# Kernel optimization log

Measured on AMD Instinct MI355X. Metric: run time of the kernel, lower is better.

Reference implementation:

```python
import jax, jax.numpy as jnp
import numpy as np

PIXEL_W = 1.0
EPS = 1e-8
BIG = 1e10


def extract_zero_crossings(s):
    """Vectorized marching-squares-style zero-crossing extraction.
    s: (H, W) SDF. Returns padded points (N, 2) float and validity mask (N,) bool,
    N = (H-1)*W + H*(W-1), in the same (vertical pairs first, then horizontal)
    order as the original python loops."""
    H, W = s.shape
    dt = s.dtype
    # vertical neighbor pairs (i, j) vs (i+1, j)
    v1, v2 = s[:-1, :], s[1:, :]
    ii = jnp.broadcast_to(jnp.arange(H - 1, dtype=dt)[:, None], (H - 1, W))
    jj = jnp.broadcast_to(jnp.arange(W, dtype=dt)[None, :], (H - 1, W))
    c1 = v1 == 0
    c2 = (~c1) & (v2 == 0)
    cx = (~c1) & (~c2) & (v1 * v2 < 0)
    alpha = jnp.abs(v1) / (jnp.abs(v1) + jnp.abs(v2) + EPS)
    row = jnp.where(c1, ii, jnp.where(c2, ii + 1.0, ii + alpha))
    pts_v = jnp.stack([row, jj], axis=-1).reshape(-1, 2)
    m_v = (c1 | c2 | cx).reshape(-1)
    # horizontal neighbor pairs (i, j) vs (i, j+1)
    h1, h2 = s[:, :-1], s[:, 1:]
    ii2 = jnp.broadcast_to(jnp.arange(H, dtype=dt)[:, None], (H, W - 1))
    jj2 = jnp.broadcast_to(jnp.arange(W - 1, dtype=dt)[None, :], (H, W - 1))
    d1 = h1 == 0
    d2 = (~d1) & (h2 == 0)
    dx = (~d1) & (~d2) & (h1 * h2 < 0)
    beta = jnp.abs(h1) / (jnp.abs(h1) + jnp.abs(h2) + EPS)
    col = jnp.where(d1, jj2, jnp.where(d2, jj2 + 1.0, jj2 + beta))
    pts_h = jnp.stack([ii2, col], axis=-1).reshape(-1, 2)
    m_h = (d1 | d2 | dx).reshape(-1)
    return jnp.concatenate([pts_v, pts_h], 0), jnp.concatenate([m_v, m_h], 0)


def pairwise_dist(p, g):
    # (Np, Ng) euclidean distances via the gram trick (avoids (Np,Ng,2) temp)
    d2 = jnp.sum(p * p, 1)[:, None] + jnp.sum(g * g, 1)[None, :] - 2.0 * (p @ g.T)
    return jnp.sqrt(jnp.maximum(d2, 0.0))


def masked_chamfer(pp, pm, gp, gm):
    # chamfer as in compute_chamfer_distance: -mean(min over gt) + mean(min over pred)
    d = pairwise_dist(pp, gp)
    d = jnp.where(pm[:, None] & gm[None, :], d, BIG)
    min_p = jnp.min(d, axis=1)
    min_g = jnp.min(d, axis=0)
    np_ = jnp.maximum(jnp.sum(pm), 1)
    ng_ = jnp.maximum(jnp.sum(gm), 1)
    return -jnp.sum(jnp.where(pm, min_p, 0.0)) / np_ + jnp.sum(jnp.where(gm, min_g, 0.0)) / ng_


def setup_inputs() -> dict:
    key = jax.random.key(0)
    k1, k2 = jax.random.split(key)
    B, H, W = 2, 80, 80
    return {
        "pred_logits": jax.random.normal(k1, (B, 1, H, W), dtype=jnp.float32),
        "gt_sdf": jax.random.normal(k2, (B, 1, H, W), dtype=jnp.float32),
    }


def reference(pred_logits, gt_sdf):
    pred = pred_logits[:, 0]  # (B, H, W)
    gt = gt_sdf[:, 0]
    pixel_loss = jnp.mean(jnp.abs(pred - gt))
    chamfers = []
    for b in range(pred.shape[0]):  # small fixed batch loop
        pp, pm = extract_zero_crossings(pred[b])
        gp, gm = extract_zero_crossings(gt[b])
        chamfers.append(masked_chamfer(pp, pm, gp, gm))
    loss = PIXEL_W * pixel_loss
    last_chamfer = jnp.mean(jnp.stack(chamfers))
    return loss, last_chamfer
```

## Files before the change

### kernel.cpp

```cpp
#include <hip/hip_runtime.h>

#define HH 80
#define WW 80
#define IMG (HH * WW)
#define NV ((HH - 1) * WW)
#define NPTS (NV + HH * (WW - 1))
#define NPIX (2 * IMG)
#define BIGF 1.0e10f
#define INVC 1.0e7f
#define EPSF 1e-8f
#define QSCALE 131072.0f

#define SETPAD 12800
#define SBLOCKS (SETPAD / 256)
#define EXBLOCKS (4 * SBLOCKS)
#define PXBLOCKS (NPIX / 256)
#define PREPB (EXBLOCKS + PXBLOCKS)

#define BLK 256
#define APT 8
#define ACHUNK (BLK * APT)
#define ABLOCKS ((NPTS + ACHUNK - 1) / ACHUNK)
#define NSLICE 32
#define MAXSLICE ((((NPTS + NSLICE - 1) / NSLICE) + 1) & ~1)

#define CNT_STRIDE 32
#define PIX_OFF 512
#define TICKET_OFF 640
#define SUM_OFF 768
#define SCALAR_BYTES 1024

__device__ __forceinline__ long long wave_reduce_ll(long long v) {
#pragma unroll
  for (int o = 32; o > 0; o >>= 1) {
    int2 p = *(int2*)&v;
    p.x = __shfl_down(p.x, o, 64);
    p.y = __shfl_down(p.y, o, 64);
    v += *(long long*)&p;
  }
  return v;
}

__global__ void k_zero(unsigned int* __restrict__ w) {
  w[threadIdx.x] = 0u;
}

__global__ void __launch_bounds__(256) k_prep(
    const float* __restrict__ pred, const float* __restrict__ gt,
    float2* __restrict__ pts, float* __restrict__ minarr,
    int* __restrict__ cnt, unsigned long long* __restrict__ pix_i) {
  __shared__ int wc[4], wo[4];
  __shared__ long long rl[4];
  int tid = threadIdx.x, lane = tid & 63, wid = tid >> 6;
  int gtid = blockIdx.x * 256 + tid;

  if (gtid < 4 * NPTS) minarr[gtid] = BIGF;

  if (blockIdx.x < EXBLOCKS) {
    int set = blockIdx.x / SBLOCKS;
    int idx = (blockIdx.x % SBLOCKS) * 256 + tid;
    const float* s = (set < 2 ? pred : gt) + (set & 1) * IMG;
    float r = 0.f, c = 0.f;
    bool valid = false;
    if (idx < NPTS) {
      if (idx < NV) {
        int i = idx / WW, j = idx - i * WW;
        float v1 = s[i * WW + j], v2 = s[(i + 1) * WW + j];
        c = (float)j;
        if (v1 == 0.f)      { r = (float)i;       valid = true; }
        else if (v2 == 0.f) { r = (float)i + 1.f; valid = true; }
        else {
          r = (float)i + fabsf(v1) / (fabsf(v1) + fabsf(v2) + EPSF);
          valid = (v1 * v2 < 0.f);
        }
      } else {
        int t = idx - NV;
        int i = t / (WW - 1), j = t - i * (WW - 1);
        float h1 = s[i * WW + j], h2 = s[i * WW + j + 1];
        r = (float)i;
        if (h1 == 0.f)      { c = (float)j;       valid = true; }
        else if (h2 == 0.f) { c = (float)j + 1.f; valid = true; }
        else {
          c = (float)j + fabsf(h1) / (fabsf(h1) + fabsf(h2) + EPSF);
          valid = (h1 * h2 < 0.f);
        }
      }
    }
    unsigned long long mask = __ballot(valid);
    int nw = __popcll(mask);
    if (lane == 0) wc[wid] = nw;
    __syncthreads();
    if (tid == 0) {
      int t0 = wc[0], t1 = wc[1], t2 = wc[2], t3 = wc[3];
      int tot = t0 + t1 + t2 + t3;
      int base = tot ? atomicAdd(&cnt[set * CNT_STRIDE], tot) : 0;
      wo[0] = base; wo[1] = base + t0; wo[2] = base + t0 + t1;
      wo[3] = base + t0 + t1 + t2;
    }
    __syncthreads();
    if (valid) {
      int lpos = __popcll(mask & ((1ull << lane) - 1ull));
      pts[set * NPTS + wo[wid] + lpos] = make_float2(r, c);
    }
  } else {
    int p = (blockIdx.x - EXBLOCKS) * 256 + tid;
    float d = fabsf(pred[p] - gt[p]);
    long long q = (long long)(d * QSCALE + 0.5f);
    q = wave_reduce_ll(q);
    if (lane == 0) rl[wid] = q;
    __syncthreads();
    if (tid == 0)
      atomicAdd(pix_i, (unsigned long long)(rl[0] + rl[1] + rl[2] + rl[3]));
  }
}

__global__ void __launch_bounds__(BLK) k_min(
    const float2* __restrict__ pts, float* __restrict__ minarr,
    const int* __restrict__ cnt) {
  int dir = blockIdx.z;
  int Aset = ((dir & 1) << 1) | (dir >> 1);
  int Bset = Aset ^ 2;
  int cntA = cnt[Aset * CNT_STRIDE], cntB = cnt[Bset * CNT_STRIDE];

  int abase0 = blockIdx.x * ACHUNK;
  if (abase0 >= cntA) return;
  int slicelen = (((cntB + NSLICE - 1) / NSLICE) + 1) & ~1;
  int b0 = blockIdx.y * slicelen;
  if (b0 >= cntB) return;
  int n = min(slicelen, cntB - b0);
  int sn = (n + 1) & ~1;

  __shared__ float4 tile[MAXSLICE];
  for (int i = threadIdx.x; i < sn; i += BLK) {
    float2 q = (i < n) ? pts[Bset * NPTS + b0 + i] : make_float2(INVC, INVC);
    tile[i] = make_float4(q.x, q.y, fmaf(q.x, q.x, q.y * q.y), 0.f);
  }
  __syncthreads();

  int abase = abase0 + threadIdx.x;
  float nx[APT], ny[APT], p2[APT], m[APT];
#pragma unroll
  for (int i = 0; i < APT; ++i) {
    int a = abase + i * BLK;
    float2 p = (a < cntA) ? pts[Aset * NPTS + a] : make_float2(0.f, 0.f);
    nx[i] = -2.f * p.x;
    ny[i] = -2.f * p.y;
    p2[i] = fmaf(p.x, p.x, p.y * p.y);
    m[i] = 3.0e38f;
  }

#pragma unroll 2
  for (int b = 0; b < sn; b += 2) {
    float4 q0 = tile[b];
    float4 q1 = tile[b + 1];
#pragma unroll
    for (int i = 0; i < APT; ++i) {
      float t0 = fmaf(ny[i], q0.y, fmaf(nx[i], q0.x, q0.z));
      float t1 = fmaf(ny[i], q1.y, fmaf(nx[i], q1.x, q1.z));
      m[i] = fminf(fminf(t0, t1), m[i]);
    }
  }

#pragma unroll
  for (int i = 0; i < APT; ++i) {
    int a = abase + i * BLK;
    if (a < cntA) {
      float d2 = fmaxf(m[i] + p2[i], 0.f);
      atomicMin((unsigned int*)&minarr[Aset * NPTS + a], __float_as_uint(d2));
    }
  }
}

__global__ void __launch_bounds__(256) k_fin(
    const float* __restrict__ minarr, const int* __restrict__ cnt,
    const unsigned long long* __restrict__ pix_i,
    unsigned long long* __restrict__ sum_i,
    unsigned int* __restrict__ ticket, float* __restrict__ out) {
  int set = blockIdx.x >> 2, q = blockIdx.x & 3;
  int tid = threadIdx.x, lane = tid & 63;
  int n = cnt[set * CNT_STRIDE];

  long long ls = 0;
  for (int i = q * 256 + tid; i < n; i += 1024) {
    float d = sqrtf(minarr[set * NPTS + i]);
    ls += (long long)(d * QSCALE + 0.5f);
  }
  ls = wave_reduce_ll(ls);
  if (lane == 0) atomicAdd(&sum_i[set], (unsigned long long)ls);
  __syncthreads();

  if (tid == 0) {
    __threadfence();
    unsigned int t = atomicAdd(ticket, 1u);
    if (t == 15u) {
      const float iq = 1.0f / QSCALE;
      float ss[4];
      for (int k = 0; k < 4; ++k)
        ss[k] = (float)((long long)atomicAdd(&sum_i[k], 0ull)) * iq;
      float n0 = fmaxf((float)cnt[0 * CNT_STRIDE], 1.f);
      float n1 = fmaxf((float)cnt[1 * CNT_STRIDE], 1.f);
      float n2 = fmaxf((float)cnt[2 * CNT_STRIDE], 1.f);
      float n3 = fmaxf((float)cnt[3 * CNT_STRIDE], 1.f);
      float ch0 = -ss[0] / n0 + ss[2] / n2;
      float ch1 = -ss[1] / n1 + ss[3] / n3;
      out[0] = (float)(long long)(*pix_i) * iq / (float)NPIX;
      out[1] = 0.5f * (ch0 + ch1);
    }
  }
}

extern "C" void kernel_launch(void* const* d_in, const int* in_sizes, int n_in,
                              void* d_out, int out_size, void* d_ws, size_t ws_size,
                              hipStream_t stream) {
  const float* pred = (const float*)d_in[0];
  const float* gt   = (const float*)d_in[1];
  float* out = (float*)d_out;

  int* cnt = (int*)d_ws;
  unsigned long long* pix_i = (unsigned long long*)((char*)d_ws + PIX_OFF);
  unsigned int* ticket = (unsigned int*)((char*)d_ws + TICKET_OFF);
  unsigned long long* sum_i = (unsigned long long*)((char*)d_ws + SUM_OFF);
  float2* pts   = (float2*)((char*)d_ws + SCALAR_BYTES);
  float* minarr = (float*)((char*)d_ws + SCALAR_BYTES + sizeof(float2) * 4 * NPTS);

  k_zero<<<1, 256, 0, stream>>>((unsigned int*)d_ws);
  k_prep<<<PREPB, 256, 0, stream>>>(pred, gt, pts, minarr, cnt, pix_i);
  k_min<<<dim3(ABLOCKS, NSLICE, 4), BLK, 0, stream>>>(pts, minarr, cnt);
  k_fin<<<16, 256, 0, stream>>>(minarr, cnt, pix_i, sum_i, ticket, out);
}
```

Baseline: 38.59 us.

## Replace atomicMin scatter with per-slice partial min rows reduced in finalize

The min kernel no longer does a global atomicMin per point. Each slice block now writes its partial squared minimum into a dedicated row, and the finalize kernel takes the min across all slice rows before summing. This removes both the minarr initialisation in prep and the atomic contention. The pixel-loss atomics are also replaced by per-block partial sums that one wave reduces in finalize, and finalize now runs 32 blocks instead of 16. The trade is extra global traffic: the finalize reads up to 32 rows per point and the workspace grows.

```diff
diff --git a/kernel.cpp b/kernel.cpp
--- a/kernel.cpp
+++ b/kernel.cpp
@@ -23,12 +23,17 @@
 #define ABLOCKS ((NPTS + ACHUNK - 1) / ACHUNK)
 #define NSLICE 32
 #define MAXSLICE ((((NPTS + NSLICE - 1) / NSLICE) + 1) & ~1)
+#define AROW 6400
+
+#define FINB 32
+#define FQ 8
 
 #define CNT_STRIDE 32
-#define PIX_OFF 512
 #define TICKET_OFF 640
 #define SUM_OFF 768
 #define SCALAR_BYTES 1024
+#define PIXPART_OFF 1024
+#define PTS_OFF 2048
 
 __device__ __forceinline__ long long wave_reduce_ll(long long v) {
 #pragma unroll
@@ -47,14 +52,11 @@
 
 __global__ void __launch_bounds__(256) k_prep(
     const float* __restrict__ pred, const float* __restrict__ gt,
-    float2* __restrict__ pts, float* __restrict__ minarr,
-    int* __restrict__ cnt, unsigned long long* __restrict__ pix_i) {
+    float2* __restrict__ pts, int* __restrict__ cnt,
+    unsigned long long* __restrict__ pixpart) {
   __shared__ int wc[4], wo[4];
   __shared__ long long rl[4];
   int tid = threadIdx.x, lane = tid & 63, wid = tid >> 6;
-  int gtid = blockIdx.x * 256 + tid;
-
-  if (gtid < 4 * NPTS) minarr[gtid] = BIGF;
 
   if (blockIdx.x < EXBLOCKS) {
     int set = blockIdx.x / SBLOCKS;
@@ -103,19 +105,20 @@
       pts[set * NPTS + wo[wid] + lpos] = make_float2(r, c);
     }
   } else {
-    int p = (blockIdx.x - EXBLOCKS) * 256 + tid;
+    int b = blockIdx.x - EXBLOCKS;
+    int p = b * 256 + tid;
     float d = fabsf(pred[p] - gt[p]);
     long long q = (long long)(d * QSCALE + 0.5f);
     q = wave_reduce_ll(q);
     if (lane == 0) rl[wid] = q;
     __syncthreads();
     if (tid == 0)
-      atomicAdd(pix_i, (unsigned long long)(rl[0] + rl[1] + rl[2] + rl[3]));
+      pixpart[b] = (unsigned long long)(rl[0] + rl[1] + rl[2] + rl[3]);
   }
 }
 
 __global__ void __launch_bounds__(BLK) k_min(
-    const float2* __restrict__ pts, float* __restrict__ minarr,
+    const float2* __restrict__ pts, float* __restrict__ minarr2,
     const int* __restrict__ cnt) {
   int dir = blockIdx.z;
   int Aset = ((dir & 1) << 1) | (dir >> 1);
@@ -161,50 +164,66 @@
     }
   }
 
+  float* row = minarr2 + (size_t)(dir * NSLICE + blockIdx.y) * AROW;
 #pragma unroll
   for (int i = 0; i < APT; ++i) {
     int a = abase + i * BLK;
-    if (a < cntA) {
-      float d2 = fmaxf(m[i] + p2[i], 0.f);
-      atomicMin((unsigned int*)&minarr[Aset * NPTS + a], __float_as_uint(d2));
-    }
+    if (a < cntA) row[a] = fmaxf(m[i] + p2[i], 0.f);
   }
 }
 
 __global__ void __launch_bounds__(256) k_fin(
-    const float* __restrict__ minarr, const int* __restrict__ cnt,
-    const unsigned long long* __restrict__ pix_i,
+    const float* __restrict__ minarr2, const int* __restrict__ cnt,
+    const unsigned long long* __restrict__ pixpart,
     unsigned long long* __restrict__ sum_i,
     unsigned int* __restrict__ ticket, float* __restrict__ out) {
-  int set = blockIdx.x >> 2, q = blockIdx.x & 3;
+  int set = blockIdx.x >> 3, q = blockIdx.x & 7;
   int tid = threadIdx.x, lane = tid & 63;
+  int dir = ((set & 1) << 1) | (set >> 1);
   int n = cnt[set * CNT_STRIDE];
+  int cntB = cnt[(set ^ 2) * CNT_STRIDE];
+  int slicelen = (((cntB + NSLICE - 1) / NSLICE) + 1) & ~1;
+  int nsv = (slicelen > 0) ? min(NSLICE, (cntB + slicelen - 1) / slicelen) : 0;
+  const float* base = minarr2 + (size_t)dir * NSLICE * AROW;
 
   long long ls = 0;
-  for (int i = q * 256 + tid; i < n; i += 1024) {
-    float d = sqrtf(minarr[set * NPTS + i]);
-    ls += (long long)(d * QSCALE + 0.5f);
+  for (int a = q * 256 + tid; a < n; a += FQ * 256) {
+    float m0 = BIGF, m1 = BIGF, m2 = BIGF, m3 = BIGF;
+    int s = 0;
+    for (; s + 4 <= nsv; s += 4) {
+      m0 = fminf(m0, base[(size_t)(s + 0) * AROW + a]);
+      m1 = fminf(m1, base[(size_t)(s + 1) * AROW + a]);
+      m2 = fminf(m2, base[(size_t)(s + 2) * AROW + a]);
+      m3 = fminf(m3, base[(size_t)(s + 3) * AROW + a]);
+    }
+    for (; s < nsv; ++s) m0 = fminf(m0, base[(size_t)s * AROW + a]);
+    float m = fminf(fminf(m0, m1), fminf(m2, m3));
+    ls += (long long)(sqrtf(m) * QSCALE + 0.5f);
   }
   ls = wave_reduce_ll(ls);
   if (lane == 0) atomicAdd(&sum_i[set], (unsigned long long)ls);
   __syncthreads();
 
-  if (tid == 0) {
-    __threadfence();
-    unsigned int t = atomicAdd(ticket, 1u);
-    if (t == 15u) {
-      const float iq = 1.0f / QSCALE;
-      float ss[4];
-      for (int k = 0; k < 4; ++k)
-        ss[k] = (float)((long long)atomicAdd(&sum_i[k], 0ull)) * iq;
-      float n0 = fmaxf((float)cnt[0 * CNT_STRIDE], 1.f);
-      float n1 = fmaxf((float)cnt[1 * CNT_STRIDE], 1.f);
-      float n2 = fmaxf((float)cnt[2 * CNT_STRIDE], 1.f);
-      float n3 = fmaxf((float)cnt[3 * CNT_STRIDE], 1.f);
-      float ch0 = -ss[0] / n0 + ss[2] / n2;
-      float ch1 = -ss[1] / n1 + ss[3] / n3;
-      out[0] = (float)(long long)(*pix_i) * iq / (float)NPIX;
-      out[1] = 0.5f * (ch0 + ch1);
+  if (tid < 64) {
+    long long pv = (lane < PXBLOCKS) ? (long long)pixpart[lane] : 0ll;
+    pv = wave_reduce_ll(pv);
+    if (lane == 0) {
+      __threadfence();
+      unsigned int t = atomicAdd(ticket, 1u);
+      if (t == FINB - 1) {
+        const float iq = 1.0f / QSCALE;
+        float ss[4];
+        for (int k = 0; k < 4; ++k)
+          ss[k] = (float)((long long)atomicAdd(&sum_i[k], 0ull)) * iq;
+        float n0 = fmaxf((float)cnt[0 * CNT_STRIDE], 1.f);
+        float n1 = fmaxf((float)cnt[1 * CNT_STRIDE], 1.f);
+        float n2 = fmaxf((float)cnt[2 * CNT_STRIDE], 1.f);
+        float n3 = fmaxf((float)cnt[3 * CNT_STRIDE], 1.f);
+        float ch0 = -ss[0] / n0 + ss[2] / n2;
+        float ch1 = -ss[1] / n1 + ss[3] / n3;
+        out[0] = (float)pv * iq / (float)NPIX;
+        out[1] = 0.5f * (ch0 + ch1);
+      }
     }
   }
 }
@@ -217,14 +236,14 @@
   float* out = (float*)d_out;
 
   int* cnt = (int*)d_ws;
-  unsigned long long* pix_i = (unsigned long long*)((char*)d_ws + PIX_OFF);
   unsigned int* ticket = (unsigned int*)((char*)d_ws + TICKET_OFF);
   unsigned long long* sum_i = (unsigned long long*)((char*)d_ws + SUM_OFF);
-  float2* pts   = (float2*)((char*)d_ws + SCALAR_BYTES);
-  float* minarr = (float*)((char*)d_ws + SCALAR_BYTES + sizeof(float2) * 4 * NPTS);
+  unsigned long long* pixpart = (unsigned long long*)((char*)d_ws + PIXPART_OFF);
+  float2* pts = (float2*)((char*)d_ws + PTS_OFF);
+  float* minarr2 = (float*)((char*)d_ws + PTS_OFF + sizeof(float2) * 4 * NPTS);
 
   k_zero<<<1, 256, 0, stream>>>((unsigned int*)d_ws);
-  k_prep<<<PREPB, 256, 0, stream>>>(pred, gt, pts, minarr, cnt, pix_i);
-  k_min<<<dim3(ABLOCKS, NSLICE, 4), BLK, 0, stream>>>(pts, minarr, cnt);
-  k_fin<<<16, 256, 0, stream>>>(minarr, cnt, pix_i, sum_i, ticket, out);
-}
+  k_prep<<<PREPB, 256, 0, stream>>>(pred, gt, pts, cnt, pixpart);
+  k_min<<<dim3(ABLOCKS, NSLICE, 4), BLK, 0, stream>>>(pts, minarr2, cnt);
+  k_fin<<<FINB, 256, 0, stream>>>(minarr2, cnt, pixpart, sum_i, ticket, out);
+}
```

Result: slower. 46.83 us (+21.4%).
